# Performance work log

Hardware: AMD Instinct MI355X
Metric: run time of the kernel (lower is better)

Reference implementation:

```python
import jax, jax.numpy as jnp
import numpy as np

EPS = 1e-7          # keras backend epsilon
BN_EPS = 1e-3       # keras BatchNormalization default epsilon
SCALES = (2, 4, 8, 16, 32)  # 2**i for i in 1..max_scale, max_scale=5


def _box_filter(x, k):
    # depthwise conv with all-ones k x k kernel, SAME padding (TF semantics)
    c = x.shape[-1]
    kern = jnp.ones((k, k, 1, c), x.dtype)
    return jax.lax.conv_general_dilated(
        x, kern, (1, 1), 'SAME',
        dimension_numbers=('NHWC', 'HWIO', 'NHWC'),
        feature_group_count=c)


def setup_inputs() -> dict:
    key = jax.random.key(0)
    ks = jax.random.split(key, 4)
    B, H, W, C, R = 16, 56, 56, 128, 8
    x = jax.random.normal(ks[0], (B, H, W, C), jnp.float32)
    kappa = jax.random.uniform(ks[1], (len(SCALES),), jnp.float32, -0.5, 0.5)
    W1 = jax.random.normal(ks[2], (C, C // R), jnp.float32) * (1.0 / np.sqrt(C))
    b1 = jnp.zeros((C // R,), jnp.float32)
    W2 = jax.random.normal(ks[3], (C // R, C), jnp.float32) * (1.0 / np.sqrt(C // R))
    b2 = jnp.zeros((C,), jnp.float32)
    gamma = jnp.ones((C,), jnp.float32)
    beta = jnp.zeros((C,), jnp.float32)
    bn_mean = jnp.zeros((C,), jnp.float32)
    bn_var = jnp.ones((C,), jnp.float32)
    return dict(x=x, kappa=kappa, W1=W1, b1=b1, W2=W2, b2=b2,
                gamma=gamma, beta=beta, bn_mean=bn_mean, bn_var=bn_var)


def reference(x, kappa, W1, b1, W2, b2, gamma, beta, bn_mean, bn_var):
    # per-sample min-max scaling over (H, W, C)
    xmin = jnp.min(x, axis=(1, 2, 3), keepdims=True)
    xmax = jnp.max(x, axis=(1, 2, 3), keepdims=True)
    xs = (x - xmin) / (xmax - xmin + EPS)

    # multi-scale box measures: [B,H,W,C,S]
    measures = jnp.stack([_box_filter(xs, k) for k in SCALES], axis=-1)
    log_m = jnp.log(measures + EPS)
    log_r = jnp.log(jnp.asarray(SCALES, jnp.float32))  # [S]

    # OLS slope of log_m vs log_r along scale axis -> alphas [B,H,W,C]
    xc = log_r - jnp.mean(log_r)
    alphas = jnp.sum(log_m * xc, axis=-1) / jnp.sum(xc * xc)

    # squeeze-and-excite on alphas
    squeeze = jnp.mean(alphas, axis=(1, 2))            # [B,C]
    hidden = jax.nn.relu(squeeze @ W1 + b1)            # [B,C//r]
    excite = jax.nn.sigmoid(hidden @ W2 + b2)          # [B,C]

    # weighted OLS estimate: alpha * (log_k + log_r) -> [B,H,W,C,S]
    k_ = jax.nn.sigmoid(kappa)
    log_k = jax.nn.sigmoid(jnp.log(k_ + EPS))          # [S]
    wols = alphas[..., None] * (log_k + log_r)

    # standardized (mean-centered) cosine similarity along scale axis, in [0,1]
    a = log_m - jnp.mean(log_m, axis=-1, keepdims=True)
    b = wols - jnp.mean(wols, axis=-1, keepdims=True)
    cos = jnp.sum(a * b, axis=-1) / (
        jnp.linalg.norm(a, axis=-1) * jnp.linalg.norm(b, axis=-1) + EPS)
    sim = 0.5 * (cos + 1.0)                            # [B,H,W,C]

    # inference-mode batchnorm on alphas
    alpha_norm = gamma * (alphas - bn_mean) * jax.lax.rsqrt(bn_var + BN_EPS) + beta

    x_exc = xs * excite[:, None, None, :]
    return sim * jax.nn.sigmoid(alpha_norm) + (1.0 - sim) * x_exc
```

## Files before the change

kernel.cpp:

```cpp
#include <hip/hip_runtime.h>
#include <hip/hip_fp16.h>

#define NTOT   6422528
#define NPERB  401408
#define HH     56
#define WW     56
#define CC     128
#define RS     7296
#define SB     415872
#define LOG2E  1.4426950408889634f

__device__ __forceinline__ float sigmoidf_fast(float x) {
    return __builtin_amdgcn_rcpf(1.f + __expf(-x));
}

__device__ __forceinline__ void kappa_consts(const float* kap, float* dcs) {
    float v[5]; float mean = 0.f;
    for (int s = 0; s < 5; s++) {
        float lr = 0.6931471805599453f * (float)(s + 1);
        float k_ = 1.f / (1.f + expf(-kap[s]));
        float lk = 1.f / (1.f + expf(-logf(k_ + 1e-7f)));
        v[s] = lk + lr; mean += v[s];
    }
    mean *= 0.2f; float nd = 0.f;
    for (int s = 0; s < 5; s++) { float d = v[s] - mean; dcs[s] = d; nd += d * d; }
    dcs[5] = sqrtf(nd);
}

__global__ void k_colsum(const float* __restrict__ x, float* __restrict__ S,
                         float* __restrict__ pmn, float* __restrict__ pmx) {
    int p = blockIdx.x;
    int b = p / 56, j = p % 56;
    int c = threadIdx.x & 127, seg = threadIdx.x >> 7;
    int xbase = b * NPERB + j * 128 + c;
    int scol  = b * SB + (j + 1) * 128 + c;
    __shared__ float tot[128];
    __shared__ float rmn[256], rmx[256];
    float mn = 3.4e38f, mx = -3.4e38f;
    float v[28];
    if (seg == 0) {
        S[scol] = 0.f;
        if (j == 0) S[b * SB + c] = 0.f;
        float acc = 0.f;
#pragma unroll
        for (int k = 0; k < 28; k++) {
            float xv = x[xbase + k * 7168];
            mn = fminf(mn, xv); mx = fmaxf(mx, xv);
            acc += xv;
            S[scol + (k + 1) * RS] = acc;
        }
        tot[c] = acc;
    } else {
        float acc = 0.f;
#pragma unroll
        for (int k = 0; k < 28; k++) {
            float xv = x[xbase + (28 + k) * 7168];
            mn = fminf(mn, xv); mx = fmaxf(mx, xv);
            acc += xv;
            v[k] = acc;
        }
    }
    __syncthreads();
    if (seg == 1) {
        float base = tot[c];
#pragma unroll
        for (int k = 0; k < 28; k++) S[scol + (29 + k) * RS] = base + v[k];
    }
    rmn[threadIdx.x] = mn; rmx[threadIdx.x] = mx;
    __syncthreads();
    for (int s = 128; s > 0; s >>= 1) {
        if (threadIdx.x < s) {
            rmn[threadIdx.x] = fminf(rmn[threadIdx.x], rmn[threadIdx.x + s]);
            rmx[threadIdx.x] = fmaxf(rmx[threadIdx.x], rmx[threadIdx.x + s]);
        }
        __syncthreads();
    }
    if (threadIdx.x == 0) { pmn[p] = rmn[0]; pmx[p] = rmx[0]; }
}

__global__ void k_rowsum(float* __restrict__ S, const float* __restrict__ kap,
                         const float* __restrict__ pmn, const float* __restrict__ pmx,
                         float* __restrict__ xmn, float* __restrict__ xiv,
                         float* __restrict__ dcs, float* __restrict__ sq) {
    int p = blockIdx.x;
    if (p == 896) {
        int t = threadIdx.x;
        for (int k = t; k < 2048; k += 256) sq[k] = 0.f;
        if (t < 16) {
            float mn = 3.4e38f, mx = -3.4e38f;
            for (int k = 0; k < 56; k++) {
                mn = fminf(mn, pmn[t * 56 + k]);
                mx = fmaxf(mx, pmx[t * 56 + k]);
            }
            xmn[t] = mn;
            xiv[t] = 1.f / (mx - mn + 1e-7f);
        } else if (t == 32) kappa_consts(kap, dcs);
        return;
    }
    int b = p / 56, i = (p % 56) + 1;
    int c = threadIdx.x & 127, seg = threadIdx.x >> 7;
    int rowbase = b * SB + i * RS + c;
    __shared__ float tot[128];
    float v[28];
    if (seg == 0) {
        S[rowbase] = 0.f;
        float acc = 0.f;
#pragma unroll
        for (int k = 0; k < 28; k++) {
            acc += S[rowbase + (k + 1) * 128];
            S[rowbase + (k + 1) * 128] = acc;
        }
        tot[c] = acc;
    } else {
        float acc = 0.f;
#pragma unroll
        for (int k = 0; k < 28; k++) {
            acc += S[rowbase + (29 + k) * 128];
            v[k] = acc;
        }
    }
    __syncthreads();
    if (seg == 1) {
        float base = tot[c];
#pragma unroll
        for (int k = 0; k < 28; k++) S[rowbase + (29 + k) * 128] = base + v[k];
    }
}

struct ScaleU { int rb1, rb0; float xmch; };

__global__ void k_gather(const float* __restrict__ S, const float* __restrict__ x,
                         const float* __restrict__ gam, const float* __restrict__ bet,
                         const float* __restrict__ bnm, const float* __restrict__ bnv,
                         const float* __restrict__ xmn, const float* __restrict__ xiv,
                         const float* __restrict__ dcs, float* __restrict__ sq,
                         unsigned int* __restrict__ ABu) {
    int p_ = blockIdx.x;
    int L  = (p_ & 7) * 448 + (p_ >> 3);
    int b = L / 224, rem = L % 224;
    int i = rem >> 2, q = rem & 3;
    int c = threadIdx.x & 127, half = threadIdx.x >> 7;
    const float* sp = S + b * SB + c;
    float g = gam[c], be = bet[c], bm = bnm[c];
    float rs = rsqrtf(bnv[c] + 1e-3f);
    float xm = xmn[b], xi = xiv[b];
    float xmxi = xm * xi;
    float A1 = g * rs, A0 = be - g * bm * rs;
    float C1 = -A1 * (LOG2E * 0.1f);
    float C0 = -A0 * LOG2E;
    float d0 = dcs[0], d1 = dcs[1], d2 = dcs[2], d3 = dcs[3], d4 = dcs[4], nd = dcs[5];

    auto mkU = [&](int hk) {
        ScaleU u;
        int y1g = min(i + hk, HH - 1) + 1;
        int y0g = max(i - hk + 1, 0);
        u.rb1 = y1g * RS; u.rb0 = y0g * RS;
        u.xmch = xm * (float)(y1g - y0g);
        return u;
    };
    ScaleU u0 = mkU(1), u1 = mkU(2), u2 = mkU(4), u3 = mkU(8), u4 = mkU(16);

    auto meas = [&](int j, const ScaleU& u, int hk) -> float {
        int x1g = min(j + hk, WW - 1) + 1;
        int x0g = max(j - hk + 1, 0);
        float cw = (float)(x1g - x0g);
        int o1 = x1g << 7, o0 = x0g << 7;
        float s = sp[u.rb1 + o1] - sp[u.rb0 + o1] - sp[u.rb1 + o0] + sp[u.rb0 + o0];
        return __log2f(fmaxf((s - u.xmch * cw) * xi, 0.f) + 1e-7f);
    };

    float asum = 0.f;
    int j0 = q * 14 + half * 7;
    for (int jj = 0; jj < 7; jj++) {
        int j = j0 + jj;
        float l0 = meas(j, u0, 1);
        float l1 = meas(j, u1, 2);
        float l2 = meas(j, u2, 4);
        float l3 = meas(j, u3, 8);
        float l4 = meas(j, u4, 16);
        float w2 = -2.f * l0 - l1 + l3 + 2.f * l4;
        asum += w2;
        float alphas = w2 * 0.1f;
        float mean = 0.2f * (l0 + l1 + l2 + l3 + l4);
        float a0 = l0 - mean, a1 = l1 - mean, a2 = l2 - mean, a3 = l3 - mean, a4 = l4 - mean;
        float na2  = a0 * a0 + a1 * a1 + a2 * a2 + a3 * a3 + a4 * a4;
        float adot = a0 * d0 + a1 * d1 + a2 * d2 + a3 * d3 + a4 * d4;
        float na = __builtin_amdgcn_sqrtf(na2);
        float cosv = (alphas * adot) * __builtin_amdgcn_rcpf(na * fabsf(alphas) * nd + 1e-7f);
        float sim = 0.5f * (cosv + 1.f);
        float sbn = __builtin_amdgcn_rcpf(1.f + exp2f(C1 * w2 + C0));
        int idx = b * NPERB + i * 7168 + j * 128 + c;
        float xs = fmaf(x[idx], xi, -xmxi);
        float A = sim * sbn;
        float B = (1.f - sim) * xs;
        __half2 h2 = __floats2half2_rn(A, B);
        ABu[idx] = __builtin_bit_cast(unsigned int, h2);
    }
    asum *= 0.1f;
    __shared__ float red[256];
    red[threadIdx.x] = asum;
    __syncthreads();
    if (threadIdx.x < 128)
        atomicAdd(&sq[b * 128 + threadIdx.x], red[threadIdx.x] + red[threadIdx.x + 128]);
}

__launch_bounds__(256)
__global__ void k_mix(const unsigned int* __restrict__ ABu, const float* __restrict__ sq,
                      const float* __restrict__ W1, const float* __restrict__ b1,
                      const float* __restrict__ W2, const float* __restrict__ b2,
                      float* __restrict__ out) {
    __shared__ float buf[2048];
    __shared__ float hid[256];
    int tid = threadIdx.x;
    for (int k = tid; k < 2048; k += 256) buf[k] = sq[k] * (1.f / 3136.f);
    __syncthreads();
    {
        int bb = tid >> 4, h = tid & 15;
        float acc = b1[h];
        for (int c2 = 0; c2 < 128; c2++) acc += buf[bb * 128 + c2] * W1[c2 * 16 + h];
        hid[bb * 16 + h] = fmaxf(acc, 0.f);
    }
    __syncthreads();
    for (int k = tid; k < 2048; k += 256) {
        int bb = k >> 7, c2 = k & 127;
        float acc = b2[c2];
#pragma unroll
        for (int h = 0; h < 16; h++) acc += hid[bb * 16 + h] * W2[h * 128 + c2];
        buf[k] = sigmoidf_fast(acc);
    }
    __syncthreads();
    for (int t = blockIdx.x * 256 + tid; t < NTOT / 4; t += 1024 * 256) {
        int flat = t * 4;
        int b = flat / NPERB, cb = flat & 127;
        uint4 u = ((const uint4*)ABu)[t];
        float2 p0 = __half22float2(__builtin_bit_cast(__half2, u.x));
        float2 p1 = __half22float2(__builtin_bit_cast(__half2, u.y));
        float2 p2 = __half22float2(__builtin_bit_cast(__half2, u.z));
        float2 p3 = __half22float2(__builtin_bit_cast(__half2, u.w));
        ((float4*)out)[t] = make_float4(p0.x + p0.y * buf[b * 128 + cb],
                                        p1.x + p1.y * buf[b * 128 + cb + 1],
                                        p2.x + p2.y * buf[b * 128 + cb + 2],
                                        p3.x + p3.y * buf[b * 128 + cb + 3]);
    }
}

extern "C" void kernel_launch(void* const* d_in, const int* in_sizes, int n_in,
                              void* d_out, int out_size, void* d_ws, size_t ws_size,
                              hipStream_t stream) {
    const float* x   = (const float*)d_in[0];
    const float* kap = (const float*)d_in[1];
    const float* W1  = (const float*)d_in[2];
    const float* b1  = (const float*)d_in[3];
    const float* W2  = (const float*)d_in[4];
    const float* b2  = (const float*)d_in[5];
    const float* gam = (const float*)d_in[6];
    const float* bet = (const float*)d_in[7];
    const float* bnm = (const float*)d_in[8];
    const float* bnv = (const float*)d_in[9];
    float* out = (float*)d_out;

    float*        S   = (float*)d_ws;
    unsigned int* ABu = (unsigned int*)(S + 16 * SB);
    float* sq  = (float*)(ABu + NTOT);
    float* pmn = sq + 2048;
    float* pmx = pmn + 1024;
    float* xmn = pmx + 1024;
    float* xiv = xmn + 16;
    float* dcs = xiv + 16;

    k_colsum<<<896, 256, 0, stream>>>(x, S, pmn, pmx);
    k_rowsum<<<897, 256, 0, stream>>>(S, kap, pmn, pmx, xmn, xiv, dcs, sq);
    k_gather<<<3584, 256, 0, stream>>>(S, x, gam, bet, bnm, bnv, xmn, xiv, dcs, sq, ABu);
    k_mix<<<1024, 256, 0, stream>>>(ABu, sq, W1, b1, W2, b2, out);
}
```

Measured before the change: 150.2 us.

## Fuse four-stage pipeline into one cooperative persistent kernel with grid syncs

Replaces the four kernel launches (column sum, row sum, gather, mix) with a single cooperative kernel of 448 blocks that uses grid-wide syncs between phases. The packed A/B half2 intermediate now stays in shared memory instead of round-tripping through global memory, and the min/max reduction and squeeze-excite run inside the same kernel. It aims to remove launch gaps and intermediate global traffic. The cost is much lower parallelism, with 448 blocks and a large shared allocation, three grid barriers, and redundant per-block excite computation. The old four-kernel path is kept as a fallback if the cooperative launch fails.

```diff
diff --git a/kernel.cpp b/kernel.cpp
--- a/kernel.cpp
+++ b/kernel.cpp
@@ -1,11 +1,13 @@
 #include <hip/hip_runtime.h>
 #include <hip/hip_fp16.h>
+#include <hip/hip_cooperative_groups.h>
+
+namespace cg = cooperative_groups;
 
 #define NTOT   6422528
 #define NPERB  401408
 #define HH     56
 #define WW     56
-#define CC     128
 #define RS     7296
 #define SB     415872
 #define LOG2E  1.4426950408889634f
@@ -25,6 +27,239 @@
     mean *= 0.2f; float nd = 0.f;
     for (int s = 0; s < 5; s++) { float d = v[s] - mean; dcs[s] = d; nd += d * d; }
     dcs[5] = sqrtf(nd);
+}
+
+struct ScaleU { int rb1, rb0; float xmch; };
+
+__launch_bounds__(256, 2)
+__global__ void k_fused(const float* __restrict__ x,   const float* __restrict__ kap,
+                        const float* __restrict__ W1,  const float* __restrict__ b1,
+                        const float* __restrict__ W2,  const float* __restrict__ b2,
+                        const float* __restrict__ gam, const float* __restrict__ bet,
+                        const float* __restrict__ bnm, const float* __restrict__ bnv,
+                        float* __restrict__ out, float* __restrict__ S,
+                        float* __restrict__ sq, float* __restrict__ pmn,
+                        float* __restrict__ pmx) {
+    cg::grid_group grid = cg::this_grid();
+    const int p = blockIdx.x;
+    const int b = p & 15;
+    const int u2 = p >> 4;
+    const int r0 = u2 * 2;
+    const int tid = threadIdx.x;
+    const int c = tid & 127, seg = tid >> 7;
+
+    __shared__ unsigned int ABs[2 * 56 * 128];
+    __shared__ float scr[512];
+    __shared__ float tot[128];
+    __shared__ float cst[9];
+    __shared__ float hid[16];
+    __shared__ float exc[128];
+
+    {
+        float mn = 3.4e38f, mx = -3.4e38f;
+        for (int jj = 0; jj < 2; jj++) {
+            const int j = r0 + jj;
+            const int xbase = b * NPERB + j * 128 + c;
+            const int scol  = b * SB + (j + 1) * 128 + c;
+            float v[28];
+            if (seg == 0) {
+                S[scol] = 0.f;
+                if (j == 0) S[b * SB + c] = 0.f;
+                float acc = 0.f;
+#pragma unroll
+                for (int k = 0; k < 28; k++) {
+                    float xv = x[xbase + k * 7168];
+                    mn = fminf(mn, xv); mx = fmaxf(mx, xv);
+                    acc += xv;
+                    S[scol + (k + 1) * RS] = acc;
+                }
+                tot[c] = acc;
+            } else {
+                float acc = 0.f;
+#pragma unroll
+                for (int k = 0; k < 28; k++) {
+                    float xv = x[xbase + (28 + k) * 7168];
+                    mn = fminf(mn, xv); mx = fmaxf(mx, xv);
+                    acc += xv;
+                    v[k] = acc;
+                }
+            }
+            __syncthreads();
+            if (seg == 1) {
+                float base = tot[c];
+#pragma unroll
+                for (int k = 0; k < 28; k++) S[scol + (29 + k) * RS] = base + v[k];
+            }
+            __syncthreads();
+        }
+        scr[tid] = mn; scr[256 + tid] = mx;
+        __syncthreads();
+        for (int s2 = 128; s2 > 0; s2 >>= 1) {
+            if (tid < s2) {
+                scr[tid]       = fminf(scr[tid],       scr[tid + s2]);
+                scr[256 + tid] = fmaxf(scr[256 + tid], scr[256 + tid + s2]);
+            }
+            __syncthreads();
+        }
+        if (tid == 0) { pmn[p] = scr[0]; pmx[p] = scr[256]; }
+        if (u2 == 0 && tid < 128) sq[b * 128 + tid] = 0.f;
+    }
+
+    grid.sync();
+
+    for (int jj = 0; jj < 2; jj++) {
+        const int i = r0 + 1 + jj;
+        const int rowbase = b * SB + i * RS + c;
+        float v[28];
+        if (seg == 0) {
+            S[rowbase] = 0.f;
+            float acc = 0.f;
+#pragma unroll
+            for (int k = 0; k < 28; k++) {
+                acc += S[rowbase + (k + 1) * 128];
+                S[rowbase + (k + 1) * 128] = acc;
+            }
+            tot[c] = acc;
+        } else {
+            float acc = 0.f;
+#pragma unroll
+            for (int k = 0; k < 28; k++) {
+                acc += S[rowbase + (29 + k) * 128];
+                v[k] = acc;
+            }
+        }
+        __syncthreads();
+        if (seg == 1) {
+            float base = tot[c];
+#pragma unroll
+            for (int k = 0; k < 28; k++) S[rowbase + (29 + k) * 128] = base + v[k];
+        }
+        __syncthreads();
+    }
+
+    grid.sync();
+
+    {
+        if (tid < 64) {
+            float mn2 = 3.4e38f, mx2 = -3.4e38f;
+            if (tid < 28) { mn2 = pmn[b + 16 * tid]; mx2 = pmx[b + 16 * tid]; }
+#pragma unroll
+            for (int off = 32; off > 0; off >>= 1) {
+                mn2 = fminf(mn2, __shfl_down(mn2, off));
+                mx2 = fmaxf(mx2, __shfl_down(mx2, off));
+            }
+            if (tid == 0) {
+                float xi = 1.f / (mx2 - mn2 + 1e-7f);
+                cst[6] = mn2; cst[7] = xi; cst[8] = mn2 * xi;
+            }
+        } else if (tid == 64) {
+            float d[6]; kappa_consts(kap, d);
+#pragma unroll
+            for (int s2 = 0; s2 < 6; s2++) cst[s2] = d[s2];
+        }
+        __syncthreads();
+
+        const float* sp = S + b * SB + c;
+        const float g = gam[c], be = bet[c], bm = bnm[c];
+        const float rsv = rsqrtf(bnv[c] + 1e-3f);
+        const float xm = cst[6], xi = cst[7], xmxi = cst[8];
+        const float A1 = g * rsv, A0 = be - g * bm * rsv;
+        const float C1 = -A1 * (LOG2E * 0.1f);
+        const float C0 = -A0 * LOG2E;
+        const float d0 = cst[0], d1 = cst[1], d2 = cst[2], d3 = cst[3], d4 = cst[4], nd = cst[5];
+
+        float asum = 0.f;
+        const int j0 = seg * 28;
+
+        for (int rr = 0; rr < 2; rr++) {
+            const int i = r0 + rr;
+
+            auto mkU = [&](int hk) {
+                ScaleU uu;
+                int y1g = min(i + hk, HH - 1) + 1;
+                int y0g = max(i - hk + 1, 0);
+                uu.rb1 = y1g * RS; uu.rb0 = y0g * RS;
+                uu.xmch = xm * (float)(y1g - y0g);
+                return uu;
+            };
+            const ScaleU u0 = mkU(1), u1 = mkU(2), u2s = mkU(4), u3 = mkU(8), u4 = mkU(16);
+
+            auto meas = [&](int j, const ScaleU& uu, int hk) -> float {
+                int x1g = min(j + hk, WW - 1) + 1;
+                int x0g = max(j - hk + 1, 0);
+                float cw = (float)(x1g - x0g);
+                int o1 = x1g << 7, o0 = x0g << 7;
+                float s = sp[uu.rb1 + o1] - sp[uu.rb0 + o1] - sp[uu.rb1 + o0] + sp[uu.rb0 + o0];
+                return __log2f(fmaxf((s - uu.xmch * cw) * xi, 0.f) + 1e-7f);
+            };
+
+            const float* xrow = x + b * NPERB + i * 7168 + c;
+            for (int jj = 0; jj < 28; jj++) {
+                int j = j0 + jj;
+                float l0 = meas(j, u0, 1);
+                float l1 = meas(j, u1, 2);
+                float l2 = meas(j, u2s, 4);
+                float l3 = meas(j, u3, 8);
+                float l4 = meas(j, u4, 16);
+                float w2 = -2.f * l0 - l1 + l3 + 2.f * l4;
+                asum += w2;
+                float alphas = w2 * 0.1f;
+                float mean = 0.2f * (l0 + l1 + l2 + l3 + l4);
+                float a0 = l0 - mean, a1 = l1 - mean, a2 = l2 - mean, a3 = l3 - mean, a4 = l4 - mean;
+                float na2  = a0 * a0 + a1 * a1 + a2 * a2 + a3 * a3 + a4 * a4;
+                float adot = a0 * d0 + a1 * d1 + a2 * d2 + a3 * d3 + a4 * d4;
+                float na = __builtin_amdgcn_sqrtf(na2);
+                float cosv = (alphas * adot) * __builtin_amdgcn_rcpf(na * fabsf(alphas) * nd + 1e-7f);
+                float sim = 0.5f * (cosv + 1.f);
+                float sbn = __builtin_amdgcn_rcpf(1.f + exp2f(C1 * w2 + C0));
+                float xs = fmaf(xrow[j * 128], xi, -xmxi);
+                float A = sim * sbn;
+                float B = (1.f - sim) * xs;
+                ABs[rr * 7168 + j * 128 + c] =
+                    __builtin_bit_cast(unsigned int, __floats2half2_rn(A, B));
+            }
+        }
+        asum *= 0.1f;
+        scr[tid] = asum;
+        __syncthreads();
+        if (tid < 128) atomicAdd(&sq[b * 128 + tid], scr[tid] + scr[tid + 128]);
+    }
+
+    grid.sync();
+
+    {
+        if (tid < 128) scr[tid] = sq[b * 128 + tid] * (1.f / 3136.f);
+        __syncthreads();
+        if (tid < 16) {
+            float acc = b1[tid];
+            for (int c2 = 0; c2 < 128; c2++) acc += scr[c2] * W1[c2 * 16 + tid];
+            hid[tid] = fmaxf(acc, 0.f);
+        }
+        __syncthreads();
+        if (tid < 128) {
+            float acc = b2[tid];
+#pragma unroll
+            for (int h = 0; h < 16; h++) acc += hid[h] * W2[h * 128 + tid];
+            exc[tid] = sigmoidf_fast(acc);
+        }
+        __syncthreads();
+        for (int rr = 0; rr < 2; rr++) {
+            const int obase4 = (b * NPERB + (r0 + rr) * 7168) >> 2;
+            const int abase  = rr * 7168;
+            for (int t = tid; t < 1792; t += 256) {
+                int j = t >> 5, c4 = (t & 31) << 2;
+                uint4 uu = *reinterpret_cast<const uint4*>(&ABs[abase + j * 128 + c4]);
+                float4 ev = *reinterpret_cast<const float4*>(&exc[c4]);
+                float2 p0 = __half22float2(__builtin_bit_cast(__half2, uu.x));
+                float2 p1 = __half22float2(__builtin_bit_cast(__half2, uu.y));
+                float2 p2 = __half22float2(__builtin_bit_cast(__half2, uu.z));
+                float2 p3 = __half22float2(__builtin_bit_cast(__half2, uu.w));
+                reinterpret_cast<float4*>(out)[obase4 + t] =
+                    make_float4(p0.x + p0.y * ev.x, p1.x + p1.y * ev.y,
+                                p2.x + p2.y * ev.z, p3.x + p3.y * ev.w);
+            }
+        }
+    }
 }
 
 __global__ void k_colsum(const float* __restrict__ x, float* __restrict__ S,
@@ -126,8 +361,6 @@
         for (int k = 0; k < 28; k++) S[rowbase + (29 + k) * 128] = base + v[k];
     }
 }
-
-struct ScaleU { int rb1, rb0; float xmch; };
 
 __global__ void k_gather(const float* __restrict__ S, const float* __restrict__ x,
                          const float* __restrict__ gam, const float* __restrict__ bet,
@@ -268,8 +501,16 @@
     float* xiv = xmn + 16;
     float* dcs = xiv + 16;
 
-    k_colsum<<<896, 256, 0, stream>>>(x, S, pmn, pmx);
-    k_rowsum<<<897, 256, 0, stream>>>(S, kap, pmn, pmx, xmn, xiv, dcs, sq);
-    k_gather<<<3584, 256, 0, stream>>>(S, x, gam, bet, bnm, bnv, xmn, xiv, dcs, sq, ABu);
-    k_mix<<<1024, 256, 0, stream>>>(ABu, sq, W1, b1, W2, b2, out);
-}
+    void* args[] = {(void*)&x, (void*)&kap, (void*)&W1, (void*)&b1, (void*)&W2,
+                    (void*)&b2, (void*)&gam, (void*)&bet, (void*)&bnm, (void*)&bnv,
+                    (void*)&out, (void*)&S, (void*)&sq, (void*)&pmn, (void*)&pmx};
+    hipError_t e = hipLaunchCooperativeKernel(reinterpret_cast<void*>(k_fused),
+                                              dim3(448), dim3(256), args, 0, stream);
+    if (e != hipSuccess) {
+        (void)hipGetLastError();
+        k_colsum<<<896, 256, 0, stream>>>(x, S, pmn, pmx);
+        k_rowsum<<<897, 256, 0, stream>>>(S, kap, pmn, pmx, xmn, xiv, dcs, sq);
+        k_gather<<<3584, 256, 0, stream>>>(S, x, gam, bet, bnm, bnv, xmn, xiv, dcs, sq, ABu);
+        k_mix<<<1024, 256, 0, stream>>>(ABu, sq, W1, b1, W2, b2, out);
+    }
+}
```

After: 340.7 us. 2.27x slower.

## Build per-channel-group summed-area tables in LDS and fuse gather

Applied to the files above, without the earlier changes.

Replaces the global summed-area-table build (column and row kernels) with one kernel that builds the SAT for 8 channels of one sample in shared memory and then computes the box measures and mixing terms from LDS. The min/max reduction becomes a separate vectorized pass using order-preserving integer atomics, and the mix kernel computes only its own sample's excitation. This removes the large global SAT write and reread and a kernel launch. In exchange there are only 256 blocks of 1024 threads with about 104KB of LDS each, so occupancy is low, and the x reads and ABu writes are 8-channel strided, which coalesces poorly.

```diff
diff --git a/kernel.cpp b/kernel.cpp
--- a/kernel.cpp
+++ b/kernel.cpp
@@ -3,15 +3,19 @@
 
 #define NTOT   6422528
 #define NPERB  401408
-#define HH     56
-#define WW     56
-#define CC     128
-#define RS     7296
-#define SB     415872
+#define NQ     100352
 #define LOG2E  1.4426950408889634f
 
 __device__ __forceinline__ float sigmoidf_fast(float x) {
     return __builtin_amdgcn_rcpf(1.f + __expf(-x));
+}
+
+__device__ __forceinline__ unsigned encf(float f) {
+    unsigned u = __float_as_uint(f);
+    return (u & 0x80000000u) ? ~u : (u | 0x80000000u);
+}
+__device__ __forceinline__ float decf(unsigned u) {
+    return __uint_as_float((u & 0x80000000u) ? (u ^ 0x80000000u) : ~u);
 }
 
 __device__ __forceinline__ void kappa_consts(const float* kap, float* dcs) {
@@ -27,220 +31,224 @@
     dcs[5] = sqrtf(nd);
 }
 
-__global__ void k_colsum(const float* __restrict__ x, float* __restrict__ S,
-                         float* __restrict__ pmn, float* __restrict__ pmx) {
+struct ScaleU { int rb1, rb0; float xmch; };
+
+__global__ void k_minmax(const float4* __restrict__ x4,
+                         unsigned* __restrict__ pmnu, unsigned* __restrict__ pmxu) {
     int p = blockIdx.x;
-    int b = p / 56, j = p % 56;
-    int c = threadIdx.x & 127, seg = threadIdx.x >> 7;
-    int xbase = b * NPERB + j * 128 + c;
-    int scol  = b * SB + (j + 1) * 128 + c;
-    __shared__ float tot[128];
+    int b = p & 15, chunk = p >> 4;
+    const float4* base = x4 + b * NQ + chunk * 3136;
+    float mn = 3.4e38f, mx = -3.4e38f;
+    for (int q = threadIdx.x; q < 3136; q += 256) {
+        float4 v = base[q];
+        mn = fminf(mn, fminf(fminf(v.x, v.y), fminf(v.z, v.w)));
+        mx = fmaxf(mx, fmaxf(fmaxf(v.x, v.y), fmaxf(v.z, v.w)));
+    }
     __shared__ float rmn[256], rmx[256];
-    float mn = 3.4e38f, mx = -3.4e38f;
+    int tid = threadIdx.x;
+    rmn[tid] = mn; rmx[tid] = mx;
+    __syncthreads();
+    for (int s = 128; s > 0; s >>= 1) {
+        if (tid < s) {
+            rmn[tid] = fminf(rmn[tid], rmn[tid + s]);
+            rmx[tid] = fmaxf(rmx[tid], rmx[tid + s]);
+        }
+        __syncthreads();
+    }
+    if (tid == 0) {
+        atomicMin(&pmnu[b], encf(rmn[0]));
+        atomicMax(&pmxu[b], encf(rmx[0]));
+    }
+}
+
+__launch_bounds__(1024)
+__global__ void k_satg(const float* __restrict__ x,   const float* __restrict__ kap,
+                       const float* __restrict__ gam, const float* __restrict__ bet,
+                       const float* __restrict__ bnm, const float* __restrict__ bnv,
+                       const unsigned* __restrict__ pmnu, const unsigned* __restrict__ pmxu,
+                       float* __restrict__ sq, unsigned int* __restrict__ ABu) {
+    __shared__ float SATl[57 * 57 * 8];
+    __shared__ float tot[448];
+    __shared__ float wsum[112];
+    __shared__ float cst[9];
+
+    const int p = blockIdx.x;
+    const int b = p & 15, cg = p >> 4;
+    const int c0 = cg * 8;
+    const int tid = threadIdx.x;
+    const int seg = (tid >= 448) ? 1 : 0;
+    const int idx = tid - seg * 448;
+    const int cc = idx & 7, lj = idx >> 3;
+    const bool act = (tid < 896);
+
+    for (int z = tid; z < 456; z += 1024) SATl[z] = 0.f;
+    for (int z = tid; z < 456; z += 1024) SATl[(z >> 3) * 456 + (z & 7)] = 0.f;
+
     float v[28];
-    if (seg == 0) {
-        S[scol] = 0.f;
-        if (j == 0) S[b * SB + c] = 0.f;
+    if (act) {
+        const float* xp = x + b * NPERB + (seg * 28) * 7168 + lj * 128 + c0 + cc;
         float acc = 0.f;
 #pragma unroll
-        for (int k = 0; k < 28; k++) {
-            float xv = x[xbase + k * 7168];
-            mn = fminf(mn, xv); mx = fmaxf(mx, xv);
-            acc += xv;
-            S[scol + (k + 1) * RS] = acc;
-        }
-        tot[c] = acc;
-    } else {
-        float acc = 0.f;
-#pragma unroll
-        for (int k = 0; k < 28; k++) {
-            float xv = x[xbase + (28 + k) * 7168];
-            mn = fminf(mn, xv); mx = fmaxf(mx, xv);
-            acc += xv;
-            v[k] = acc;
-        }
-    }
-    __syncthreads();
-    if (seg == 1) {
-        float base = tot[c];
-#pragma unroll
-        for (int k = 0; k < 28; k++) S[scol + (29 + k) * RS] = base + v[k];
-    }
-    rmn[threadIdx.x] = mn; rmx[threadIdx.x] = mx;
-    __syncthreads();
-    for (int s = 128; s > 0; s >>= 1) {
-        if (threadIdx.x < s) {
-            rmn[threadIdx.x] = fminf(rmn[threadIdx.x], rmn[threadIdx.x + s]);
-            rmx[threadIdx.x] = fmaxf(rmx[threadIdx.x], rmx[threadIdx.x + s]);
-        }
-        __syncthreads();
-    }
-    if (threadIdx.x == 0) { pmn[p] = rmn[0]; pmx[p] = rmx[0]; }
-}
-
-__global__ void k_rowsum(float* __restrict__ S, const float* __restrict__ kap,
-                         const float* __restrict__ pmn, const float* __restrict__ pmx,
-                         float* __restrict__ xmn, float* __restrict__ xiv,
-                         float* __restrict__ dcs, float* __restrict__ sq) {
+        for (int k = 0; k < 28; k++) { acc += xp[k * 7168]; v[k] = acc; }
+        if (seg == 0) {
+#pragma unroll
+            for (int k = 0; k < 28; k++) SATl[(k + 1) * 456 + (lj + 1) * 8 + cc] = v[k];
+            tot[idx] = acc;
+        }
+    }
+    __syncthreads();
+    if (act && seg == 1) {
+        float basev = tot[idx];
+#pragma unroll
+        for (int k = 0; k < 28; k++) SATl[(k + 29) * 456 + (lj + 1) * 8 + cc] = basev + v[k];
+    }
+    if (tid == 896) {
+        float d[6]; kappa_consts(kap, d);
+        for (int s2 = 0; s2 < 6; s2++) cst[s2] = d[s2];
+    } else if (tid == 897) {
+        float mnv = decf(pmnu[b]), mxv = decf(pmxu[b]);
+        float xi = 1.f / (mxv - mnv + 1e-7f);
+        cst[6] = mnv; cst[7] = xi; cst[8] = mnv * xi;
+    }
+    __syncthreads();
+
+    if (act) {
+        const int colbase = (lj + 1) * 456 + cc;
+#pragma unroll
+        for (int k = 0; k < 28; k++) v[k] = SATl[colbase + (seg * 28 + 1 + k) * 8];
+#pragma unroll
+        for (int k = 1; k < 28; k++) v[k] += v[k - 1];
+        if (seg == 0) {
+#pragma unroll
+            for (int k = 0; k < 28; k++) SATl[colbase + (1 + k) * 8] = v[k];
+            tot[idx] = v[27];
+        }
+    }
+    __syncthreads();
+    if (act && seg == 1) {
+        const int colbase = (lj + 1) * 456 + cc;
+        float basev = tot[idx];
+#pragma unroll
+        for (int k = 0; k < 28; k++) SATl[colbase + (29 + k) * 8] = basev + v[k];
+    }
+    __syncthreads();
+
+    float asum = 0.f;
+    if (act) {
+        const int i = lj;
+        const int j0 = seg * 28;
+        const float xm = cst[6], xi = cst[7], xmxi = cst[8];
+        const int ci = c0 + cc;
+        const float g = gam[ci], be = bet[ci], bm = bnm[ci];
+        const float rsv = rsqrtf(bnv[ci] + 1e-3f);
+        const float A1c = g * rsv, A0c = be - g * bm * rsv;
+        const float C1 = -A1c * (LOG2E * 0.1f);
+        const float C0 = -A0c * LOG2E;
+        const float d0 = cst[0], d1 = cst[1], d2 = cst[2], d3 = cst[3], d4 = cst[4], nd = cst[5];
+        const float* sp = SATl + cc;
+
+        auto mkU = [&](int hk) {
+            ScaleU uu;
+            int y1g = min(i + hk, 55) + 1;
+            int y0g = max(i - hk + 1, 0);
+            uu.rb1 = y1g * 456; uu.rb0 = y0g * 456;
+            uu.xmch = xm * (float)(y1g - y0g);
+            return uu;
+        };
+        const ScaleU u0 = mkU(1), u1 = mkU(2), u2 = mkU(4), u3 = mkU(8), u4 = mkU(16);
+
+        auto meas = [&](int j, const ScaleU& uu, int hk) -> float {
+            int x1g = min(j + hk, 55) + 1;
+            int x0g = max(j - hk + 1, 0);
+            float cw = (float)(x1g - x0g);
+            int o1 = x1g << 3, o0 = x0g << 3;
+            float s = sp[uu.rb1 + o1] - sp[uu.rb0 + o1] - sp[uu.rb1 + o0] + sp[uu.rb0 + o0];
+            return __log2f(fmaxf((s - uu.xmch * cw) * xi, 0.f) + 1e-7f);
+        };
+
+        const float* xrow = x + b * NPERB + i * 7168 + c0 + cc;
+        unsigned int* abrow = ABu + b * NPERB + i * 7168 + c0 + cc;
+        for (int jj = 0; jj < 28; jj++) {
+            int j = j0 + jj;
+            float l0 = meas(j, u0, 1);
+            float l1 = meas(j, u1, 2);
+            float l2 = meas(j, u2, 4);
+            float l3 = meas(j, u3, 8);
+            float l4 = meas(j, u4, 16);
+            float w2 = -2.f * l0 - l1 + l3 + 2.f * l4;
+            asum += w2;
+            float alphas = w2 * 0.1f;
+            float mean = 0.2f * (l0 + l1 + l2 + l3 + l4);
+            float a0 = l0 - mean, a1 = l1 - mean, a2 = l2 - mean, a3 = l3 - mean, a4 = l4 - mean;
+            float na2  = a0 * a0 + a1 * a1 + a2 * a2 + a3 * a3 + a4 * a4;
+            float adot = a0 * d0 + a1 * d1 + a2 * d2 + a3 * d3 + a4 * d4;
+            float na = __builtin_amdgcn_sqrtf(na2);
+            float cosv = (alphas * adot) * __builtin_amdgcn_rcpf(na * fabsf(alphas) * nd + 1e-7f);
+            float sim = 0.5f * (cosv + 1.f);
+            float sbn = __builtin_amdgcn_rcpf(1.f + exp2f(C1 * w2 + C0));
+            float xs = fmaf(xrow[j * 128], xi, -xmxi);
+            float A = sim * sbn;
+            float B = (1.f - sim) * xs;
+            abrow[j * 128] = __builtin_bit_cast(unsigned int, __floats2half2_rn(A, B));
+        }
+    }
+    asum += __shfl_down(asum, 32);
+    asum += __shfl_down(asum, 16);
+    asum += __shfl_down(asum, 8);
+    {
+        int w = tid >> 6, l = tid & 63;
+        if (w < 14 && l < 8) wsum[w * 8 + l] = asum;
+    }
+    __syncthreads();
+    if (tid < 8) {
+        float s = 0.f;
+#pragma unroll
+        for (int w = 0; w < 14; w++) s += wsum[w * 8 + tid];
+        atomicAdd(&sq[b * 128 + c0 + tid], s * 0.1f);
+    }
+}
+
+__launch_bounds__(256)
+__global__ void k_mix2(const unsigned int* __restrict__ ABu, const float* __restrict__ sq,
+                       const float* __restrict__ W1, const float* __restrict__ b1,
+                       const float* __restrict__ W2, const float* __restrict__ b2,
+                       float* __restrict__ out) {
+    __shared__ float sqz[128];
+    __shared__ float hid[16];
+    __shared__ float exc[128];
     int p = blockIdx.x;
-    if (p == 896) {
-        int t = threadIdx.x;
-        for (int k = t; k < 2048; k += 256) sq[k] = 0.f;
-        if (t < 16) {
-            float mn = 3.4e38f, mx = -3.4e38f;
-            for (int k = 0; k < 56; k++) {
-                mn = fminf(mn, pmn[t * 56 + k]);
-                mx = fmaxf(mx, pmx[t * 56 + k]);
-            }
-            xmn[t] = mn;
-            xiv[t] = 1.f / (mx - mn + 1e-7f);
-        } else if (t == 32) kappa_consts(kap, dcs);
-        return;
-    }
-    int b = p / 56, i = (p % 56) + 1;
-    int c = threadIdx.x & 127, seg = threadIdx.x >> 7;
-    int rowbase = b * SB + i * RS + c;
-    __shared__ float tot[128];
-    float v[28];
-    if (seg == 0) {
-        S[rowbase] = 0.f;
-        float acc = 0.f;
-#pragma unroll
-        for (int k = 0; k < 28; k++) {
-            acc += S[rowbase + (k + 1) * 128];
-            S[rowbase + (k + 1) * 128] = acc;
-        }
-        tot[c] = acc;
-    } else {
-        float acc = 0.f;
-#pragma unroll
-        for (int k = 0; k < 28; k++) {
-            acc += S[rowbase + (29 + k) * 128];
-            v[k] = acc;
-        }
-    }
-    __syncthreads();
-    if (seg == 1) {
-        float base = tot[c];
-#pragma unroll
-        for (int k = 0; k < 28; k++) S[rowbase + (29 + k) * 128] = base + v[k];
-    }
-}
-
-struct ScaleU { int rb1, rb0; float xmch; };
-
-__global__ void k_gather(const float* __restrict__ S, const float* __restrict__ x,
-                         const float* __restrict__ gam, const float* __restrict__ bet,
-                         const float* __restrict__ bnm, const float* __restrict__ bnv,
-                         const float* __restrict__ xmn, const float* __restrict__ xiv,
-                         const float* __restrict__ dcs, float* __restrict__ sq,
-                         unsigned int* __restrict__ ABu) {
-    int p_ = blockIdx.x;
-    int L  = (p_ & 7) * 448 + (p_ >> 3);
-    int b = L / 224, rem = L % 224;
-    int i = rem >> 2, q = rem & 3;
-    int c = threadIdx.x & 127, half = threadIdx.x >> 7;
-    const float* sp = S + b * SB + c;
-    float g = gam[c], be = bet[c], bm = bnm[c];
-    float rs = rsqrtf(bnv[c] + 1e-3f);
-    float xm = xmn[b], xi = xiv[b];
-    float xmxi = xm * xi;
-    float A1 = g * rs, A0 = be - g * bm * rs;
-    float C1 = -A1 * (LOG2E * 0.1f);
-    float C0 = -A0 * LOG2E;
-    float d0 = dcs[0], d1 = dcs[1], d2 = dcs[2], d3 = dcs[3], d4 = dcs[4], nd = dcs[5];
-
-    auto mkU = [&](int hk) {
-        ScaleU u;
-        int y1g = min(i + hk, HH - 1) + 1;
-        int y0g = max(i - hk + 1, 0);
-        u.rb1 = y1g * RS; u.rb0 = y0g * RS;
-        u.xmch = xm * (float)(y1g - y0g);
-        return u;
-    };
-    ScaleU u0 = mkU(1), u1 = mkU(2), u2 = mkU(4), u3 = mkU(8), u4 = mkU(16);
-
-    auto meas = [&](int j, const ScaleU& u, int hk) -> float {
-        int x1g = min(j + hk, WW - 1) + 1;
-        int x0g = max(j - hk + 1, 0);
-        float cw = (float)(x1g - x0g);
-        int o1 = x1g << 7, o0 = x0g << 7;
-        float s = sp[u.rb1 + o1] - sp[u.rb0 + o1] - sp[u.rb1 + o0] + sp[u.rb0 + o0];
-        return __log2f(fmaxf((s - u.xmch * cw) * xi, 0.f) + 1e-7f);
-    };
-
-    float asum = 0.f;
-    int j0 = q * 14 + half * 7;
-    for (int jj = 0; jj < 7; jj++) {
-        int j = j0 + jj;
-        float l0 = meas(j, u0, 1);
-        float l1 = meas(j, u1, 2);
-        float l2 = meas(j, u2, 4);
-        float l3 = meas(j, u3, 8);
-        float l4 = meas(j, u4, 16);
-        float w2 = -2.f * l0 - l1 + l3 + 2.f * l4;
-        asum += w2;
-        float alphas = w2 * 0.1f;
-        float mean = 0.2f * (l0 + l1 + l2 + l3 + l4);
-        float a0 = l0 - mean, a1 = l1 - mean, a2 = l2 - mean, a3 = l3 - mean, a4 = l4 - mean;
-        float na2  = a0 * a0 + a1 * a1 + a2 * a2 + a3 * a3 + a4 * a4;
-        float adot = a0 * d0 + a1 * d1 + a2 * d2 + a3 * d3 + a4 * d4;
-        float na = __builtin_amdgcn_sqrtf(na2);
-        float cosv = (alphas * adot) * __builtin_amdgcn_rcpf(na * fabsf(alphas) * nd + 1e-7f);
-        float sim = 0.5f * (cosv + 1.f);
-        float sbn = __builtin_amdgcn_rcpf(1.f + exp2f(C1 * w2 + C0));
-        int idx = b * NPERB + i * 7168 + j * 128 + c;
-        float xs = fmaf(x[idx], xi, -xmxi);
-        float A = sim * sbn;
-        float B = (1.f - sim) * xs;
-        __half2 h2 = __floats2half2_rn(A, B);
-        ABu[idx] = __builtin_bit_cast(unsigned int, h2);
-    }
-    asum *= 0.1f;
-    __shared__ float red[256];
-    red[threadIdx.x] = asum;
-    __syncthreads();
-    if (threadIdx.x < 128)
-        atomicAdd(&sq[b * 128 + threadIdx.x], red[threadIdx.x] + red[threadIdx.x + 128]);
-}
-
-__launch_bounds__(256)
-__global__ void k_mix(const unsigned int* __restrict__ ABu, const float* __restrict__ sq,
-                      const float* __restrict__ W1, const float* __restrict__ b1,
-                      const float* __restrict__ W2, const float* __restrict__ b2,
-                      float* __restrict__ out) {
-    __shared__ float buf[2048];
-    __shared__ float hid[256];
+    int b = p & 15, chunk = p >> 4;
     int tid = threadIdx.x;
-    for (int k = tid; k < 2048; k += 256) buf[k] = sq[k] * (1.f / 3136.f);
-    __syncthreads();
-    {
-        int bb = tid >> 4, h = tid & 15;
-        float acc = b1[h];
-        for (int c2 = 0; c2 < 128; c2++) acc += buf[bb * 128 + c2] * W1[c2 * 16 + h];
-        hid[bb * 16 + h] = fmaxf(acc, 0.f);
-    }
-    __syncthreads();
-    for (int k = tid; k < 2048; k += 256) {
-        int bb = k >> 7, c2 = k & 127;
-        float acc = b2[c2];
-#pragma unroll
-        for (int h = 0; h < 16; h++) acc += hid[bb * 16 + h] * W2[h * 128 + c2];
-        buf[k] = sigmoidf_fast(acc);
-    }
-    __syncthreads();
-    for (int t = blockIdx.x * 256 + tid; t < NTOT / 4; t += 1024 * 256) {
-        int flat = t * 4;
-        int b = flat / NPERB, cb = flat & 127;
-        uint4 u = ((const uint4*)ABu)[t];
+    if (tid < 128) sqz[tid] = sq[b * 128 + tid] * (1.f / 3136.f);
+    __syncthreads();
+    if (tid < 16) {
+        float acc = b1[tid];
+        for (int c2 = 0; c2 < 128; c2++) acc += sqz[c2] * W1[c2 * 16 + tid];
+        hid[tid] = fmaxf(acc, 0.f);
+    }
+    __syncthreads();
+    if (tid < 128) {
+        float acc = b2[tid];
+#pragma unroll
+        for (int h = 0; h < 16; h++) acc += hid[h] * W2[h * 128 + tid];
+        exc[tid] = sigmoidf_fast(acc);
+    }
+    __syncthreads();
+    const uint4* ab4 = (const uint4*)ABu;
+    float4* out4 = (float4*)out;
+    const int base = b * NQ + chunk * 1568;
+    for (int q = tid; q < 1568; q += 256) {
+        int g = base + q;
+        int cb = (g & 31) << 2;
+        uint4 u = ab4[g];
         float2 p0 = __half22float2(__builtin_bit_cast(__half2, u.x));
         float2 p1 = __half22float2(__builtin_bit_cast(__half2, u.y));
         float2 p2 = __half22float2(__builtin_bit_cast(__half2, u.z));
         float2 p3 = __half22float2(__builtin_bit_cast(__half2, u.w));
-        ((float4*)out)[t] = make_float4(p0.x + p0.y * buf[b * 128 + cb],
-                                        p1.x + p1.y * buf[b * 128 + cb + 1],
-                                        p2.x + p2.y * buf[b * 128 + cb + 2],
-                                        p3.x + p3.y * buf[b * 128 + cb + 3]);
+        out4[g] = make_float4(p0.x + p0.y * exc[cb],
+                              p1.x + p1.y * exc[cb + 1],
+                              p2.x + p2.y * exc[cb + 2],
+                              p3.x + p3.y * exc[cb + 3]);
     }
 }
 
@@ -259,17 +267,16 @@
     const float* bnv = (const float*)d_in[9];
     float* out = (float*)d_out;
 
-    float*        S   = (float*)d_ws;
-    unsigned int* ABu = (unsigned int*)(S + 16 * SB);
-    float* sq  = (float*)(ABu + NTOT);
-    float* pmn = sq + 2048;
-    float* pmx = pmn + 1024;
-    float* xmn = pmx + 1024;
-    float* xiv = xmn + 16;
-    float* dcs = xiv + 16;
-
-    k_colsum<<<896, 256, 0, stream>>>(x, S, pmn, pmx);
-    k_rowsum<<<897, 256, 0, stream>>>(S, kap, pmn, pmx, xmn, xiv, dcs, sq);
-    k_gather<<<3584, 256, 0, stream>>>(S, x, gam, bet, bnm, bnv, xmn, xiv, dcs, sq, ABu);
-    k_mix<<<1024, 256, 0, stream>>>(ABu, sq, W1, b1, W2, b2, out);
-}
+    float*    sq   = (float*)d_ws;
+    unsigned* pmnu = (unsigned*)(sq + 2048);
+    unsigned* pmxu = pmnu + 16;
+    unsigned* ABu  = (unsigned*)(pmxu + 16);
+
+    hipMemsetAsync(sq, 0, 2048 * sizeof(float), stream);
+    hipMemsetAsync(pmnu, 0xFF, 16 * sizeof(unsigned), stream);
+    hipMemsetAsync(pmxu, 0x00, 16 * sizeof(unsigned), stream);
+
+    k_minmax<<<512, 256, 0, stream>>>((const float4*)x, pmnu, pmxu);
+    k_satg<<<256, 1024, 0, stream>>>(x, kap, gam, bet, bnm, bnv, pmnu, pmxu, sq, ABu);
+    k_mix2<<<1024, 256, 0, stream>>>(ABu, sq, W1, b1, W2, b2, out);
+}
```

Result: no change. 149.8 us (-0.3%).
